# Performance work log

Measured on AMD Instinct MI355X. Metric: run time of the kernel, lower is better.

Reference implementation:

```python
import jax, jax.numpy as jnp
import numpy as np

B, L, S, T_IP = 2, 4096, 77, 16
C, C_CROSS, H = 1280, 768, 20
DH = C // H
REGION_WEIGHT = 0.3  # scalar inside weight_func: bias = region_state * sigma * REGION_WEIGHT
IP_SCALE = 1.0


def setup_inputs() -> dict:
    key = jax.random.key(0)
    ks = jax.random.split(key, 11)
    def w(k, shape, s=0.02):
        return jax.random.normal(k, shape, dtype=jnp.float32) * s
    return {
        "hidden_states": jax.random.normal(ks[0], (B, L, C), dtype=jnp.float32),
        "encoder_hidden_states": jax.random.normal(ks[1], (B, S, C_CROSS), dtype=jnp.float32),
        "ip_hidden_states": jax.random.normal(ks[2], (B, T_IP, C_CROSS), dtype=jnp.float32),
        "region_state": jax.random.uniform(ks[3], (B, L, S), dtype=jnp.float32),
        "sigma": jnp.full((1,), 14.6, dtype=jnp.float32),
        "Wq": w(ks[4], (C, C)),
        "Wk": w(ks[5], (C_CROSS, C)),
        "Wv": w(ks[6], (C_CROSS, C)),
        "Wk_ip": w(ks[7], (C_CROSS, C)),
        "Wv_ip": w(ks[8], (C_CROSS, C)),
        "Wout": w(ks[9], (C, C)),
        "b_out": jnp.zeros((C,), dtype=jnp.float32),
    }


def _split_heads(x):
    # [B, T, C] -> [B, H, T, DH]
    b, t, _ = x.shape
    return x.reshape(b, t, H, DH).transpose(0, 2, 1, 3)


def reference(hidden_states, encoder_hidden_states, ip_hidden_states, region_state,
              sigma, Wq, Wk, Wv, Wk_ip, Wv_ip, Wout, b_out):
    residual = hidden_states
    scale = 1.0 / np.sqrt(DH).astype(np.float32)

    q = _split_heads(hidden_states @ Wq)            # [B,H,L,DH]
    k = _split_heads(encoder_hidden_states @ Wk)    # [B,H,S,DH]
    v = _split_heads(encoder_hidden_states @ Wv)    # [B,H,S,DH]

    # region-state-biased cross attention (manual softmax path)
    scores = jnp.einsum('bhld,bhsd->bhls', q, k) * scale  # [B,H,L,S]
    # weight_func(region_state, sigma, attn_weight) -> region_state * sigma * REGION_WEIGHT,
    # broadcast over heads (repeat_interleave B -> B*H in the original).
    bias = (region_state * sigma[0] * REGION_WEIGHT)[:, None, :, :]  # [B,1,L,S]
    attn = jax.nn.softmax(scores + bias, axis=-1)
    out = jnp.einsum('bhls,bhsd->bhld', attn, v)
    out = out.transpose(0, 2, 1, 3).reshape(B, L, C)

    # IP-adapter stream: standard SDPA against image-prompt tokens
    k_ip = _split_heads(ip_hidden_states @ Wk_ip)   # [B,H,T,DH]
    v_ip = _split_heads(ip_hidden_states @ Wv_ip)
    s_ip = jax.nn.softmax(jnp.einsum('bhld,bhtd->bhlt', q, k_ip) * scale, axis=-1)
    out_ip = jnp.einsum('bhlt,bhtd->bhld', s_ip, v_ip).transpose(0, 2, 1, 3).reshape(B, L, C)

    out = out + IP_SCALE * out_ip
    out = out @ Wout + b_out     # attn.to_out[0]; to_out[1] is dropout (identity at p=0)
    return out + residual
```

## Files before the change

kernel.cpp:

```cpp
#include <hip/hip_runtime.h>
#include <cstdint>
#include <cstddef>

#define B_   2
#define L_   4096
#define S_   77
#define TIP_ 16
#define C_   1280
#define CC_  768
#define H_   20

typedef unsigned short u16;
typedef unsigned int   u32;
typedef __attribute__((ext_vector_type(8))) short bf16x8;
typedef __attribute__((ext_vector_type(8))) unsigned short u16x8;
typedef __attribute__((ext_vector_type(4))) float f32x4;

#define GEMM_SMEM (2*128*64*2 + 2*160*64*2)

__device__ __forceinline__ u16 f2bf(float x) {
  u32 u = __float_as_uint(x);
  u32 r = (u + 0x7fffu + ((u >> 16) & 1u)) >> 16;
  return (u16)r;
}

__device__ __forceinline__ void gload16(const u16* g, const u16* l) {
  __builtin_amdgcn_global_load_lds(
      (const __attribute__((address_space(1))) u32*)g,
      (__attribute__((address_space(3))) u32*)(uintptr_t)l, 16, 0, 0);
}

__device__ __forceinline__ void wg_barrier() {
  asm volatile("s_barrier" ::: "memory");
}
template<int N>
__device__ __forceinline__ void vm_wait() {
  asm volatile("s_waitcnt vmcnt(%0)" :: "i"(N) : "memory");
}

__global__ __launch_bounds__(256) void prep_all(
    const float* __restrict__ X, const float* __restrict__ enc, const float* __restrict__ ip,
    u16* __restrict__ Xbf, u16* __restrict__ encbf, u16* __restrict__ ipbf,
    const float* __restrict__ Wq,  const float* __restrict__ Wk,   const float* __restrict__ Wv,
    const float* __restrict__ Wkip,const float* __restrict__ Wvip,
    u16* __restrict__ WqT, u16* __restrict__ WkT, u16* __restrict__ WvT,
    u16* __restrict__ WkipT, u16* __restrict__ WvipT) {
  __shared__ float tile[32][33];
  const int bid = blockIdx.x;
  if (bid < 2048) {
    const int nX = B_*L_*C_;
    const int nE = B_*S_*CC_;
    const int nI = B_*TIP_*CC_;
    const int total4 = (nX + nE + nI) >> 2;
    for (int i = bid*256 + threadIdx.x; i < total4; i += 2048*256) {
      int idx = i << 2;
      const float* src; u16* dst; int off;
      if (idx < nX)            { src = X;   dst = Xbf;   off = idx; }
      else if (idx < nX + nE)  { src = enc; dst = encbf; off = idx - nX; }
      else                     { src = ip;  dst = ipbf;  off = idx - nX - nE; }
      float4 v = *(const float4*)(src + off);
      ushort4 o;
      o.x = f2bf(v.x); o.y = f2bf(v.y); o.z = f2bf(v.z); o.w = f2bf(v.w);
      *(ushort4*)(dst + off) = o;
    }
    return;
  }
  int t = bid - 2048;
  const float* src; u16* dst; int K;
  if      (t < 1600) { src = Wq;   dst = WqT;   K = C_;  }
  else if (t < 2560) { src = Wk;   dst = WkT;   K = CC_; t -= 1600; }
  else if (t < 3520) { src = Wv;   dst = WvT;   K = CC_; t -= 2560; }
  else if (t < 4480) { src = Wkip; dst = WkipT; K = CC_; t -= 3520; }
  else               { src = Wvip; dst = WvipT; K = CC_; t -= 4480; }
  const int tileK = t / 40, tileN = t % 40;
  const int tx = threadIdx.x & 31, ty = threadIdx.x >> 5;
  const int k0 = tileK*32, n0 = tileN*32;
  #pragma unroll
  for (int r = 0; r < 32; r += 8)
    tile[ty + r][tx] = src[(size_t)(k0 + ty + r)*C_ + n0 + tx];
  __syncthreads();
  #pragma unroll
  for (int r = 0; r < 32; r += 8) {
    const int n = n0 + ty + r, k = k0 + tx;
    dst[(size_t)n*K + k] = f2bf(tile[tx][ty + r]);
  }
}

template<int MODE, typename OutT>
__device__ __forceinline__ void gemm_core(
    char* smem,
    const u16* __restrict__ A, int lda, int M,
    const u16* __restrict__ BT, int K,
    OutT* __restrict__ Cm,
    const float* __restrict__ bias, const float* __restrict__ resid,
    int mt, int nt) {
  u16* AsB = (u16*)smem;
  u16* BsB = (u16*)(smem + 2*128*64*2);
  const int tid  = threadIdx.x;
  const int lane = tid & 63, wave = tid >> 6;
  const int wr = wave >> 1, wc = wave & 1;
  const int lhi = lane >> 4, llo = lane & 15;
  const int lsw = llo & 7;

  f32x4 acc[2][5] = {};

  auto stage = [&](int kt) {
    u16* Asb = AsB + (kt & 1)*(128*64);
    u16* Bsb = BsB + (kt & 1)*(160*64);
    #pragma unroll
    for (int it = 0; it < 2; ++it) {
      const int chunk = it*512 + wave*64 + lane;
      const int r = chunk >> 3, c8 = chunk & 7;
      const int g8 = c8 ^ (r & 7);
      int row_g = mt*128 + r; row_g = (row_g < M) ? row_g : (M - 1);
      gload16(A + (size_t)row_g*lda + kt*64 + g8*8,
              Asb + (size_t)(it*512 + wave*64)*8);
    }
    #pragma unroll
    for (int it = 0; it < 2; ++it) {
      const int chunk = it*512 + wave*64 + lane;
      const int r = chunk >> 3, c8 = chunk & 7;
      const int g8 = c8 ^ (r & 7);
      const int nrow = nt*160 + r;
      gload16(BT + (size_t)nrow*K + kt*64 + g8*8,
              Bsb + (size_t)(it*512 + wave*64)*8);
    }
    { const int chunk = 1024 + (wave & 3)*64 + lane;
      const int r = chunk >> 3, c8 = chunk & 7;
      const int g8 = c8 ^ (r & 7);
      const int nrow = nt*160 + r;
      gload16(BT + (size_t)nrow*K + kt*64 + g8*8,
              Bsb + (size_t)(1024 + (wave & 3)*64)*8);
    }
  };

  auto compute = [&](int kt) {
    const u16* Asb = AsB + (kt & 1)*(128*64);
    const u16* Bsb = BsB + (kt & 1)*(160*64);
    #pragma unroll
    for (int ks = 0; ks < 2; ++ks) {
      bf16x8 av[2], bv[5];
      #pragma unroll
      for (int mm = 0; mm < 2; ++mm) {
        const int row = wr*32 + mm*16 + llo;
        av[mm] = *(const bf16x8*)(Asb + row*64 + (((ks*4 + lhi) ^ lsw) << 3));
      }
      #pragma unroll
      for (int nn = 0; nn < 5; ++nn) {
        const int row = wc*80 + nn*16 + llo;
        bv[nn] = *(const bf16x8*)(Bsb + row*64 + (((ks*4 + lhi) ^ lsw) << 3));
      }
      __builtin_amdgcn_s_setprio(1);
      #pragma unroll
      for (int mm = 0; mm < 2; ++mm)
        #pragma unroll
        for (int nn = 0; nn < 5; ++nn)
          acc[mm][nn] = __builtin_amdgcn_mfma_f32_16x16x32_bf16(av[mm], bv[nn], acc[mm][nn], 0, 0, 0);
      __builtin_amdgcn_s_setprio(0);
    }
  };

  const int nkt = K >> 6;
  stage(0);
  stage(1);
  vm_wait<5>();
  wg_barrier();
  __builtin_amdgcn_sched_barrier(0);

  for (int kt = 0; kt < nkt; ++kt) {
    compute(kt);
    if (kt + 2 < nkt) {
      wg_barrier();
      stage(kt + 2);
      vm_wait<5>();
      wg_barrier();
      __builtin_amdgcn_sched_barrier(0);
    } else if (kt + 1 < nkt) {
      vm_wait<0>();
      wg_barrier();
      __builtin_amdgcn_sched_barrier(0);
    }
  }

  #pragma unroll
  for (int mm = 0; mm < 2; ++mm) {
    #pragma unroll
    for (int nn = 0; nn < 5; ++nn) {
      const int row0 = mt*128 + wr*32 + mm*16 + lhi*4;
      const int col  = nt*160 + wc*80 + nn*16 + llo;
      #pragma unroll
      for (int r = 0; r < 4; ++r) {
        const int row = row0 + r;
        if (row < M) {
          float v = acc[mm][nn][r];
          if constexpr (MODE == 1) {
            v += bias[col] + resid[(size_t)row*C_ + col];
            Cm[(size_t)row*C_ + col] = v;
          } else {
            Cm[(size_t)row*C_ + col] = f2bf(v);
          }
        }
      }
    }
  }
}

__global__ __launch_bounds__(512, 4) void gemm_qkv(
    const u16* __restrict__ Xbf, const u16* __restrict__ WqT, u16* __restrict__ Qbf,
    const u16* __restrict__ encbf, const u16* __restrict__ ipbf,
    const u16* __restrict__ WkT, const u16* __restrict__ WvT,
    const u16* __restrict__ WkipT, const u16* __restrict__ WvipT,
    u16* __restrict__ Kbf, u16* __restrict__ Vbf,
    u16* __restrict__ Kipbf, u16* __restrict__ Vipbf,
    const float* __restrict__ Wout, u16* __restrict__ WoutT) {
  __shared__ char smem[GEMM_SMEM];
  const int bid = blockIdx.x;
  if (bid < 512) {
    const int swz = (bid & 7) * 64 + (bid >> 3);
    gemm_core<2, u16>(smem, Xbf, C_, B_*L_, WqT, C_, Qbf, nullptr, nullptr, swz >> 3, swz & 7);
    return;
  }
  if (bid < 560) {
    const int t = bid - 512;
    const int zr = t >> 3, nt = t & 7;
    const u16* A; const u16* BT; u16* Cm; int M, mt;
    switch (zr) {
      case 0: A = encbf; BT = WkT;   Cm = Kbf;   M = B_*S_;   mt = 0; break;
      case 1: A = encbf; BT = WkT;   Cm = Kbf;   M = B_*S_;   mt = 1; break;
      case 2: A = encbf; BT = WvT;   Cm = Vbf;   M = B_*S_;   mt = 0; break;
      case 3: A = encbf; BT = WvT;   Cm = Vbf;   M = B_*S_;   mt = 1; break;
      case 4: A = ipbf;  BT = WkipT; Cm = Kipbf; M = B_*TIP_; mt = 0; break;
      default:A = ipbf;  BT = WvipT; Cm = Vipbf; M = B_*TIP_; mt = 0; break;
    }
    gemm_core<2, u16>(smem, A, CC_, M, BT, CC_, Cm, nullptr, nullptr, mt, nt);
    return;
  }
  const int half = threadIdx.x >> 8;
  const int ht   = threadIdx.x & 255;
  const int t2   = (bid - 560)*2 + half;
  float (*tile)[33] = (float(*)[33])(smem + half*4352);
  const int tileK = t2 / 40, tileN = t2 % 40;
  const int tx = ht & 31, ty = ht >> 5;
  const int k0 = tileK*32, n0 = tileN*32;
  #pragma unroll
  for (int r = 0; r < 32; r += 8)
    tile[ty + r][tx] = Wout[(size_t)(k0 + ty + r)*C_ + n0 + tx];
  __syncthreads();
  #pragma unroll
  for (int r = 0; r < 32; r += 8) {
    const int n = n0 + ty + r, k = k0 + tx;
    WoutT[(size_t)n*C_ + k] = f2bf(tile[tx][ty + r]);
  }
}

__global__ __launch_bounds__(512, 4) void gemm_out(
    const u16* __restrict__ A, const u16* __restrict__ BT,
    float* __restrict__ Cm, const float* __restrict__ bias, const float* __restrict__ resid) {
  __shared__ char smem[GEMM_SMEM];
  const int bid = blockIdx.x;
  const int swz = (bid & 7) * 64 + (bid >> 3);
  gemm_core<1, float>(smem, A, C_, B_*L_, BT, C_, Cm, bias, resid, swz >> 3, swz & 7);
}

#define KSP   96
#define KLD   72
#define PLD   100
__global__ __launch_bounds__(256) void attn_mfma(
    const u16* __restrict__ Qbf,
    const u16* __restrict__ Kbf,  const u16* __restrict__ Vbf,
    const u16* __restrict__ Kipbf, const u16* __restrict__ Vipbf,
    const float* __restrict__ region, const float* __restrict__ sigma,
    u16* __restrict__ attnbf) {
  __shared__ u16 Vt[64*PLD];
  __shared__ u16 R2[128*PLD];
  u16* Kl = R2;
  u16* Pl = R2;
  const int b = blockIdx.z, h = blockIdx.y;
  const int tid = threadIdx.x, lane = tid & 63, wave = tid >> 6;
  const int llo = lane & 15, lhi = lane >> 4;

  for (int i = tid; i < KSP*8; i += 256) {
    const int r = i >> 3, c8 = i & 7;
    u16x8 val = {0,0,0,0,0,0,0,0};
    if (r < S_)
      val = *(const u16x8*)(Kbf + ((size_t)(b*S_ + r))*C_ + h*64 + c8*8);
    else if (r >= 80)
      val = *(const u16x8*)(Kipbf + ((size_t)(b*TIP_ + r - 80))*C_ + h*64 + c8*8);
    *(u16x8*)(Kl + r*KLD + c8*8) = val;
  }
  for (int c = tid; c < KSP*8; c += 256) {
    const int s = c >> 3, d0 = (c & 7) * 8;
    u16x8 v = {0,0,0,0,0,0,0,0};
    if (s < S_)
      v = *(const u16x8*)(Vbf + ((size_t)(b*S_ + s))*C_ + h*64 + d0);
    else if (s >= 80)
      v = *(const u16x8*)(Vipbf + ((size_t)(b*TIP_ + s - 80))*C_ + h*64 + d0);
    #pragma unroll
    for (int j = 0; j < 8; ++j)
      Vt[(d0 + j)*PLD + s] = v[j];
  }
  __syncthreads();

  const int row0 = blockIdx.x*128 + wave*32;

  bf16x8 av[2][2];
  #pragma unroll
  for (int mm = 0; mm < 2; ++mm)
    #pragma unroll
    for (int ks = 0; ks < 2; ++ks)
      av[mm][ks] = *(const bf16x8*)(Qbf + ((size_t)(b*L_ + row0 + mm*16 + llo))*C_ + h*64 + ks*32 + lhi*8);

  f32x4 acc[2][6] = {};
  #pragma unroll
  for (int ks = 0; ks < 2; ++ks) {
    bf16x8 bv[6];
    #pragma unroll
    for (int nn = 0; nn < 6; ++nn)
      bv[nn] = *(const bf16x8*)(Kl + (nn*16 + llo)*KLD + ks*32 + lhi*8);
    #pragma unroll
    for (int mm = 0; mm < 2; ++mm)
      #pragma unroll
      for (int nn = 0; nn < 6; ++nn)
        acc[mm][nn] = __builtin_amdgcn_mfma_f32_16x16x32_bf16(av[mm][ks], bv[nn], acc[mm][nn], 0, 0, 0);
  }
  __syncthreads();

  const float sigscale = sigma[0] * 0.3f;
  const float scale = 0.125f;
  u16* Pw = Pl + wave*32*PLD;

  #pragma unroll
  for (int mm = 0; mm < 2; ++mm) {
    const int rowbase = b*L_ + row0 + mm*16 + lhi*4;
    float sc[5][4];
    float mx[4] = {-1e30f, -1e30f, -1e30f, -1e30f};
    #pragma unroll
    for (int nn = 0; nn < 5; ++nn) {
      const int col = nn*16 + llo;
      #pragma unroll
      for (int r = 0; r < 4; ++r) {
        float v = -1e30f;
        if (col < S_) {
          const float bias = region[((size_t)(rowbase + r))*S_ + col] * sigscale;
          v = fmaf(acc[mm][nn][r], scale, bias);
        }
        sc[nn][r] = v;
        mx[r] = fmaxf(mx[r], v);
      }
    }
    #pragma unroll
    for (int st = 1; st < 16; st <<= 1)
      #pragma unroll
      for (int r = 0; r < 4; ++r)
        mx[r] = fmaxf(mx[r], __shfl_xor(mx[r], st));
    float sum[4] = {0.f, 0.f, 0.f, 0.f};
    #pragma unroll
    for (int nn = 0; nn < 5; ++nn)
      #pragma unroll
      for (int r = 0; r < 4; ++r) {
        const float e = __expf(sc[nn][r] - mx[r]);
        sc[nn][r] = e; sum[r] += e;
      }
    #pragma unroll
    for (int st = 1; st < 16; st <<= 1)
      #pragma unroll
      for (int r = 0; r < 4; ++r)
        sum[r] += __shfl_xor(sum[r], st);
    float inv[4];
    #pragma unroll
    for (int r = 0; r < 4; ++r) inv[r] = 1.f / sum[r];

    float ipe[4], mi[4], sumi[4];
    #pragma unroll
    for (int r = 0; r < 4; ++r) { ipe[r] = acc[mm][5][r] * scale; mi[r] = ipe[r]; }
    #pragma unroll
    for (int st = 1; st < 16; st <<= 1)
      #pragma unroll
      for (int r = 0; r < 4; ++r)
        mi[r] = fmaxf(mi[r], __shfl_xor(mi[r], st));
    #pragma unroll
    for (int r = 0; r < 4; ++r) { ipe[r] = __expf(ipe[r] - mi[r]); sumi[r] = ipe[r]; }
    #pragma unroll
    for (int st = 1; st < 16; st <<= 1)
      #pragma unroll
      for (int r = 0; r < 4; ++r)
        sumi[r] += __shfl_xor(sumi[r], st);

    #pragma unroll
    for (int nn = 0; nn < 5; ++nn)
      #pragma unroll
      for (int r = 0; r < 4; ++r)
        Pw[(mm*16 + lhi*4 + r)*PLD + nn*16 + llo] = f2bf(sc[nn][r] * inv[r]);
    #pragma unroll
    for (int r = 0; r < 4; ++r)
      Pw[(mm*16 + lhi*4 + r)*PLD + 80 + llo] = f2bf(ipe[r] / sumi[r]);
  }

  f32x4 oacc[2][4] = {};
  #pragma unroll
  for (int ks = 0; ks < 3; ++ks) {
    bf16x8 pa[2], vv[4];
    #pragma unroll
    for (int mm = 0; mm < 2; ++mm)
      pa[mm] = *(const bf16x8*)(Pw + (mm*16 + llo)*PLD + ks*32 + lhi*8);
    #pragma unroll
    for (int nn = 0; nn < 4; ++nn)
      vv[nn] = *(const bf16x8*)(Vt + (nn*16 + llo)*PLD + ks*32 + lhi*8);
    #pragma unroll
    for (int mm = 0; mm < 2; ++mm)
      #pragma unroll
      for (int nn = 0; nn < 4; ++nn)
        oacc[mm][nn] = __builtin_amdgcn_mfma_f32_16x16x32_bf16(pa[mm], vv[nn], oacc[mm][nn], 0, 0, 0);
  }

  #pragma unroll
  for (int mm = 0; mm < 2; ++mm)
    #pragma unroll
    for (int nn = 0; nn < 4; ++nn)
      #pragma unroll
      for (int r = 0; r < 4; ++r) {
        const int grow = row0 + mm*16 + lhi*4 + r;
        attnbf[((size_t)(b*L_ + grow))*C_ + h*64 + nn*16 + llo] = f2bf(oacc[mm][nn][r]);
      }
}

extern "C" void kernel_launch(void* const* d_in, const int* in_sizes, int n_in,
                              void* d_out, int out_size, void* d_ws, size_t ws_size,
                              hipStream_t stream) {
  const float* hidden = (const float*)d_in[0];
  const float* enc    = (const float*)d_in[1];
  const float* ip     = (const float*)d_in[2];
  const float* region = (const float*)d_in[3];
  const float* sigma  = (const float*)d_in[4];
  const float* Wq     = (const float*)d_in[5];
  const float* Wk     = (const float*)d_in[6];
  const float* Wv     = (const float*)d_in[7];
  const float* Wkip   = (const float*)d_in[8];
  const float* Wvip   = (const float*)d_in[9];
  const float* Wout   = (const float*)d_in[10];
  const float* bout   = (const float*)d_in[11];

  char* base = (char*)d_ws;
  size_t off = 0;
  auto carve = [&](size_t bytes) -> void* {
    void* r = base + off;
    off += (bytes + 255) & ~(size_t)255;
    return r;
  };
  u16* Xbf    = (u16*)carve((size_t)B_*L_*C_*2);
  u16* encbf  = (u16*)carve((size_t)B_*S_*CC_*2);
  u16* ipbf   = (u16*)carve((size_t)B_*TIP_*CC_*2);
  u16* WqT    = (u16*)carve((size_t)C_*C_*2);
  u16* WkT    = (u16*)carve((size_t)C_*CC_*2);
  u16* WvT    = (u16*)carve((size_t)C_*CC_*2);
  u16* WkipT  = (u16*)carve((size_t)C_*CC_*2);
  u16* WvipT  = (u16*)carve((size_t)C_*CC_*2);
  u16* WoutT  = (u16*)carve((size_t)C_*C_*2);
  u16* Qbf    = (u16*)carve((size_t)B_*L_*C_*2);
  u16* Kbf    = (u16*)carve((size_t)B_*S_*C_*2);
  u16* Vbf    = (u16*)carve((size_t)B_*S_*C_*2);
  u16* Kipbf  = (u16*)carve((size_t)B_*TIP_*C_*2);
  u16* Vipbf  = (u16*)carve((size_t)B_*TIP_*C_*2);
  u16* attnbf = (u16*)carve((size_t)B_*L_*C_*2);
  (void)ws_size; (void)in_sizes; (void)n_in; (void)out_size;

  prep_all<<<dim3(2048 + 5440), 256, 0, stream>>>(
      hidden, enc, ip, Xbf, encbf, ipbf,
      Wq, Wk, Wv, Wkip, Wvip,
      WqT, WkT, WvT, WkipT, WvipT);
  gemm_qkv<<<dim3(1360), 512, 0, stream>>>(Xbf, WqT, Qbf,
                                           encbf, ipbf, WkT, WvT, WkipT, WvipT,
                                           Kbf, Vbf, Kipbf, Vipbf,
                                           Wout, WoutT);
  attn_mfma<<<dim3(L_/128, H_, B_), 256, 0, stream>>>(Qbf, Kbf, Vbf, Kipbf, Vipbf,
                                                      region, sigma, attnbf);
  gemm_out<<<dim3(512), 512, 0, stream>>>(attnbf, WoutT, (float*)d_out, bout, hidden);
}
```

Before: 125.0 us.

## Load GEMM A operand directly into registers instead of staging through LDS

```diff
diff --git a/kernel.cpp b/kernel.cpp
--- a/kernel.cpp
+++ b/kernel.cpp
@@ -16,7 +16,7 @@
 typedef __attribute__((ext_vector_type(8))) unsigned short u16x8;
 typedef __attribute__((ext_vector_type(4))) float f32x4;
 
-#define GEMM_SMEM (2*128*64*2 + 2*160*64*2)
+#define GEMM_SMEM (2*160*64*2)
 
 __device__ __forceinline__ u16 f2bf(float x) {
   u32 u = __float_as_uint(x);
@@ -94,8 +94,7 @@
     OutT* __restrict__ Cm,
     const float* __restrict__ bias, const float* __restrict__ resid,
     int mt, int nt) {
-  u16* AsB = (u16*)smem;
-  u16* BsB = (u16*)(smem + 2*128*64*2);
+  u16* BsB = (u16*)smem;
   const int tid  = threadIdx.x;
   const int lane = tid & 63, wave = tid >> 6;
   const int wr = wave >> 1, wc = wave & 1;
@@ -104,18 +103,8 @@
 
   f32x4 acc[2][5] = {};
 
-  auto stage = [&](int kt) {
-    u16* Asb = AsB + (kt & 1)*(128*64);
+  auto bstage = [&](int kt) {
     u16* Bsb = BsB + (kt & 1)*(160*64);
-    #pragma unroll
-    for (int it = 0; it < 2; ++it) {
-      const int chunk = it*512 + wave*64 + lane;
-      const int r = chunk >> 3, c8 = chunk & 7;
-      const int g8 = c8 ^ (r & 7);
-      int row_g = mt*128 + r; row_g = (row_g < M) ? row_g : (M - 1);
-      gload16(A + (size_t)row_g*lda + kt*64 + g8*8,
-              Asb + (size_t)(it*512 + wave*64)*8);
-    }
     #pragma unroll
     for (int it = 0; it < 2; ++it) {
       const int chunk = it*512 + wave*64 + lane;
@@ -134,17 +123,27 @@
     }
   };
 
-  auto compute = [&](int kt) {
-    const u16* Asb = AsB + (kt & 1)*(128*64);
+  const u16* arow[2];
+  #pragma unroll
+  for (int mm = 0; mm < 2; ++mm) {
+    int row = mt*128 + wr*32 + mm*16 + llo;
+    row = (row < M) ? row : (M - 1);
+    arow[mm] = A + (size_t)row*lda;
+  }
+
+  auto aload = [&](int kt, bf16x8 av[2][2]) {
+    #pragma unroll
+    for (int mm = 0; mm < 2; ++mm)
+      #pragma unroll
+      for (int ks = 0; ks < 2; ++ks)
+        av[mm][ks] = *(const bf16x8*)(arow[mm] + kt*64 + ks*32 + lhi*8);
+  };
+
+  auto compute = [&](int kt, const bf16x8 av[2][2]) {
     const u16* Bsb = BsB + (kt & 1)*(160*64);
     #pragma unroll
     for (int ks = 0; ks < 2; ++ks) {
-      bf16x8 av[2], bv[5];
-      #pragma unroll
-      for (int mm = 0; mm < 2; ++mm) {
-        const int row = wr*32 + mm*16 + llo;
-        av[mm] = *(const bf16x8*)(Asb + row*64 + (((ks*4 + lhi) ^ lsw) << 3));
-      }
+      bf16x8 bv[5];
       #pragma unroll
       for (int nn = 0; nn < 5; ++nn) {
         const int row = wc*80 + nn*16 + llo;
@@ -155,28 +154,37 @@
       for (int mm = 0; mm < 2; ++mm)
         #pragma unroll
         for (int nn = 0; nn < 5; ++nn)
-          acc[mm][nn] = __builtin_amdgcn_mfma_f32_16x16x32_bf16(av[mm], bv[nn], acc[mm][nn], 0, 0, 0);
+          acc[mm][nn] = __builtin_amdgcn_mfma_f32_16x16x32_bf16(av[mm][ks], bv[nn], acc[mm][nn], 0, 0, 0);
       __builtin_amdgcn_s_setprio(0);
     }
   };
 
   const int nkt = K >> 6;
-  stage(0);
-  stage(1);
-  vm_wait<5>();
+  bf16x8 avA[2][2], avB[2][2];
+  bstage(0); bstage(1);
+  aload(0, avA); aload(1, avB);
+  vm_wait<11>();
   wg_barrier();
   __builtin_amdgcn_sched_barrier(0);
 
-  for (int kt = 0; kt < nkt; ++kt) {
-    compute(kt);
+  for (int kt = 0; kt < nkt; kt += 2) {
+    compute(kt, avA);
+    wg_barrier();
     if (kt + 2 < nkt) {
+      bstage(kt + 2);
+      aload(kt + 2, avA);
+      vm_wait<7>();
+    } else {
+      vm_wait<0>();
+    }
+    wg_barrier();
+    __builtin_amdgcn_sched_barrier(0);
+    compute(kt + 1, avB);
+    if (kt + 3 < nkt) {
       wg_barrier();
-      stage(kt + 2);
-      vm_wait<5>();
-      wg_barrier();
-      __builtin_amdgcn_sched_barrier(0);
-    } else if (kt + 1 < nkt) {
-      vm_wait<0>();
+      bstage(kt + 3);
+      aload(kt + 3, avB);
+      vm_wait<7>();
       wg_barrier();
       __builtin_amdgcn_sched_barrier(0);
     }
```

After: 199.7 us. +59.7%, slower.

## Switch projection GEMMs to 256x256 tiles with interleaved half-tile pipelining

Applied to the files above, without the earlier changes.

```diff
diff --git a/kernel.cpp b/kernel.cpp
--- a/kernel.cpp
+++ b/kernel.cpp
@@ -16,7 +16,9 @@
 typedef __attribute__((ext_vector_type(8))) unsigned short u16x8;
 typedef __attribute__((ext_vector_type(4))) float f32x4;
 
-#define GEMM_SMEM (2*128*64*2 + 2*160*64*2)
+#define SMEM_BYTES (2*2*128*64*2 * 2)
+#define HALF_U16   (128*64)
+#define TILE_U16   (2*HALF_U16)
 
 __device__ __forceinline__ u16 f2bf(float x) {
   u32 u = __float_as_uint(x);
@@ -87,6 +89,150 @@
 }
 
 template<int MODE, typename OutT>
+__device__ __forceinline__ void gemm256_core(
+    char* smem,
+    const u16* __restrict__ A, int lda, int M,
+    const u16* __restrict__ BT, int K,
+    OutT* __restrict__ Cm,
+    const float* __restrict__ bias, const float* __restrict__ resid,
+    int mt, int nt) {
+  u16* Als = (u16*)smem;
+  u16* Bls = (u16*)(smem + 2*TILE_U16*2);
+  const int tid  = threadIdx.x;
+  const int lane = tid & 63, wave = tid >> 6;
+  const int wr = wave >> 2, wc = wave & 3;
+  const int lhi = lane >> 4, llo = lane & 15;
+  const int lsw = llo & 7;
+  const int nkt = K >> 6;
+
+  f32x4 acc[8][4] = {};
+
+  auto stage_half = [&](int t, int isB, int h) {
+    if (t >= nkt) return;
+    u16* dst = (isB ? Bls : Als) + (t & 1)*TILE_U16 + h*HALF_U16;
+    #pragma unroll
+    for (int it = 0; it < 2; ++it) {
+      const int chunk = it*512 + tid;
+      const int r = chunk >> 3, c8 = chunk & 7;
+      const int g8 = c8 ^ (r & 7);
+      const u16* src;
+      if (isB) {
+        const int nrow = nt*256 + h*128 + r;
+        src = BT + (size_t)nrow*K + t*64 + g8*8;
+      } else {
+        int mrow = mt*256 + h*128 + r; mrow = (mrow < M) ? mrow : (M - 1);
+        src = A + (size_t)mrow*lda + t*64 + g8*8;
+      }
+      gload16(src, dst + (size_t)chunk*8);
+    }
+  };
+
+  auto read_av = [&](int t, int mi, bf16x8 av[4][2]) {
+    const u16* Ah = Als + (t & 1)*TILE_U16 + wr*HALF_U16;
+    #pragma unroll
+    for (int j = 0; j < 4; ++j) {
+      const int r = (mi*4 + j)*16 + llo;
+      #pragma unroll
+      for (int ks = 0; ks < 2; ++ks)
+        av[j][ks] = *(const bf16x8*)(Ah + r*64 + (((ks*4 + lhi) ^ lsw) << 3));
+    }
+  };
+  auto read_bv = [&](int t, int ni, bf16x8 bv[2][2]) {
+    const u16* Bh = Bls + (t & 1)*TILE_U16 + (wc >> 1)*HALF_U16;
+    #pragma unroll
+    for (int j = 0; j < 2; ++j) {
+      const int r = (wc & 1)*64 + (ni*2 + j)*16 + llo;
+      #pragma unroll
+      for (int ks = 0; ks < 2; ++ks)
+        bv[j][ks] = *(const bf16x8*)(Bh + r*64 + (((ks*4 + lhi) ^ lsw) << 3));
+    }
+  };
+  auto mfma16 = [&](int mi, int ni, bf16x8 av[4][2], bf16x8 bv[2][2]) {
+    __builtin_amdgcn_s_setprio(1);
+    #pragma unroll
+    for (int j = 0; j < 4; ++j)
+      #pragma unroll
+      for (int jj = 0; jj < 2; ++jj)
+        #pragma unroll
+        for (int ks = 0; ks < 2; ++ks)
+          acc[mi*4 + j][ni*2 + jj] =
+              __builtin_amdgcn_mfma_f32_16x16x32_bf16(av[j][ks], bv[jj][ks],
+                                                      acc[mi*4 + j][ni*2 + jj], 0, 0, 0);
+    __builtin_amdgcn_s_setprio(0);
+  };
+
+  stage_half(0, 0, 0); stage_half(0, 1, 0);
+  stage_half(0, 0, 1); stage_half(0, 1, 1);
+  stage_half(1, 0, 0); stage_half(1, 1, 0);
+  vm_wait<4>();
+  wg_barrier();
+  __builtin_amdgcn_sched_barrier(0);
+
+  const int niter = nkt >> 1;
+  for (int i = 0; i < niter; ++i) {
+    const int ta = 2*i, tb = ta + 1, ta2 = ta + 2, tb2 = tb + 2;
+    bf16x8 av0[4][2], av1[4][2], bv0[2][2], bv1[2][2];
+    stage_half(tb, 0, 1);
+    read_av(ta, 0, av0); read_bv(ta, 0, bv0);
+    mfma16(0, 0, av0, bv0);
+    wg_barrier();
+    stage_half(tb, 1, 1);
+    read_av(ta, 1, av1);
+    mfma16(1, 0, av1, bv0);
+    wg_barrier();
+    stage_half(ta2, 0, 0);
+    read_bv(ta, 1, bv1);
+    mfma16(0, 1, av0, bv1);
+    wg_barrier();
+    stage_half(ta2, 1, 0);
+    mfma16(1, 1, av1, bv1);
+    if (ta2 < nkt) vm_wait<4>();
+    else           vm_wait<0>();
+    wg_barrier();
+    __builtin_amdgcn_sched_barrier(0);
+    stage_half(ta2, 0, 1);
+    read_av(tb, 0, av0); read_bv(tb, 0, bv0);
+    mfma16(0, 0, av0, bv0);
+    wg_barrier();
+    stage_half(ta2, 1, 1);
+    read_av(tb, 1, av1);
+    mfma16(1, 0, av1, bv0);
+    wg_barrier();
+    stage_half(tb2, 0, 0);
+    read_bv(tb, 1, bv1);
+    mfma16(0, 1, av0, bv1);
+    wg_barrier();
+    stage_half(tb2, 1, 0);
+    mfma16(1, 1, av1, bv1);
+    if (tb2 < nkt) vm_wait<4>();
+    wg_barrier();
+    __builtin_amdgcn_sched_barrier(0);
+  }
+
+  #pragma unroll
+  for (int mf = 0; mf < 8; ++mf) {
+    #pragma unroll
+    for (int nf = 0; nf < 4; ++nf) {
+      const int row0 = mt*256 + wr*128 + mf*16 + lhi*4;
+      const int col  = nt*256 + wc*64 + nf*16 + llo;
+      #pragma unroll
+      for (int r = 0; r < 4; ++r) {
+        const int row = row0 + r;
+        if (row < M) {
+          float v = acc[mf][nf][r];
+          if constexpr (MODE == 1) {
+            v += bias[col] + resid[(size_t)row*C_ + col];
+            Cm[(size_t)row*C_ + col] = v;
+          } else {
+            Cm[(size_t)row*C_ + col] = f2bf(v);
+          }
+        }
+      }
+    }
+  }
+}
+
+template<int MODE, typename OutT>
 __device__ __forceinline__ void gemm_core(
     char* smem,
     const u16* __restrict__ A, int lda, int M,
@@ -205,7 +351,7 @@
   }
 }
 
-__global__ __launch_bounds__(512, 4) void gemm_qkv(
+__global__ __launch_bounds__(512, 2) void gemm_qkv(
     const u16* __restrict__ Xbf, const u16* __restrict__ WqT, u16* __restrict__ Qbf,
     const u16* __restrict__ encbf, const u16* __restrict__ ipbf,
     const u16* __restrict__ WkT, const u16* __restrict__ WvT,
@@ -213,15 +359,16 @@
     u16* __restrict__ Kbf, u16* __restrict__ Vbf,
     u16* __restrict__ Kipbf, u16* __restrict__ Vipbf,
     const float* __restrict__ Wout, u16* __restrict__ WoutT) {
-  __shared__ char smem[GEMM_SMEM];
+  __shared__ char smem[SMEM_BYTES];
   const int bid = blockIdx.x;
-  if (bid < 512) {
-    const int swz = (bid & 7) * 64 + (bid >> 3);
-    gemm_core<2, u16>(smem, Xbf, C_, B_*L_, WqT, C_, Qbf, nullptr, nullptr, swz >> 3, swz & 7);
+  if (bid < 160) {
+    const int swz = (bid & 7) * 20 + (bid >> 3);
+    gemm256_core<2, u16>(smem, Xbf, C_, B_*L_, WqT, C_, Qbf, nullptr, nullptr,
+                         swz / 5, swz % 5);
     return;
   }
-  if (bid < 560) {
-    const int t = bid - 512;
+  if (bid < 208) {
+    const int t = bid - 160;
     const int zr = t >> 3, nt = t & 7;
     const u16* A; const u16* BT; u16* Cm; int M, mt;
     switch (zr) {
@@ -237,7 +384,7 @@
   }
   const int half = threadIdx.x >> 8;
   const int ht   = threadIdx.x & 255;
-  const int t2   = (bid - 560)*2 + half;
+  const int t2   = (bid - 208)*2 + half;
   float (*tile)[33] = (float(*)[33])(smem + half*4352);
   const int tileK = t2 / 40, tileN = t2 % 40;
   const int tx = ht & 31, ty = ht >> 5;
@@ -253,13 +400,14 @@
   }
 }
 
-__global__ __launch_bounds__(512, 4) void gemm_out(
+__global__ __launch_bounds__(512, 2) void gemm_out(
     const u16* __restrict__ A, const u16* __restrict__ BT,
     float* __restrict__ Cm, const float* __restrict__ bias, const float* __restrict__ resid) {
-  __shared__ char smem[GEMM_SMEM];
+  __shared__ char smem[SMEM_BYTES];
   const int bid = blockIdx.x;
-  const int swz = (bid & 7) * 64 + (bid >> 3);
-  gemm_core<1, float>(smem, A, C_, B_*L_, BT, C_, Cm, bias, resid, swz >> 3, swz & 7);
+  const int swz = (bid & 7) * 20 + (bid >> 3);
+  gemm256_core<1, float>(smem, A, C_, B_*L_, BT, C_, Cm, bias, resid,
+                         swz / 5, swz % 5);
 }
 
 #define KSP   96
@@ -468,11 +616,11 @@
       hidden, enc, ip, Xbf, encbf, ipbf,
       Wq, Wk, Wv, Wkip, Wvip,
       WqT, WkT, WvT, WkipT, WvipT);
-  gemm_qkv<<<dim3(1360), 512, 0, stream>>>(Xbf, WqT, Qbf,
+  gemm_qkv<<<dim3(1008), 512, 0, stream>>>(Xbf, WqT, Qbf,
                                            encbf, ipbf, WkT, WvT, WkipT, WvipT,
                                            Kbf, Vbf, Kipbf, Vipbf,
                                            Wout, WoutT);
   attn_mfma<<<dim3(L_/128, H_, B_), 256, 0, stream>>>(Qbf, Kbf, Vbf, Kipbf, Vipbf,
                                                       region, sigma, attnbf);
-  gemm_out<<<dim3(512), 512, 0, stream>>>(attnbf, WoutT, (float*)d_out, bout, hidden);
-}
+  gemm_out<<<dim3(160), 512, 0, stream>>>(attnbf, WoutT, (float*)d_out, bout, hidden);
+}
```

Result: slower. 153.0 us (+22.4%).
